# Performance work log

Measured on AMD Instinct MI355X. Metric: run time of the kernel, lower is better.

The kernel has to match this reference:

```python
import jax, jax.numpy as jnp
import numpy as np

N, IN, HID, HEADS, HC, E, K = 50000, 512, 256, 8, 32, 600000, 4
EPS = 1e-5


def _gcn(h_in, W, b, src, dst):
    # PyG GCNConv: add self-loops, symmetric normalization, linear + bias
    h = h_in @ W  # [N, out]
    loop = jnp.arange(N)
    s = jnp.concatenate([src, loop])
    d = jnp.concatenate([dst, loop])
    deg = jax.ops.segment_sum(jnp.ones(s.shape[0], h.dtype), d, num_segments=N)
    dinv = jnp.where(deg > 0, jax.lax.rsqrt(deg), 0.0)
    msg = h[s] * (dinv[s] * dinv[d])[:, None]
    return jax.ops.segment_sum(msg, d, num_segments=N) + b


def _gat(h_in, W, a_src, a_dst, b, src, dst):
    # PyG GATConv: self-loops, LeakyReLU(0.2) logits, per-dst softmax, concat heads
    loop = jnp.arange(N)
    s = jnp.concatenate([src, loop])
    d = jnp.concatenate([dst, loop])
    h = (h_in @ W).reshape(N, HEADS, HC)
    e = jax.nn.leaky_relu((h * a_src).sum(-1)[s] + (h * a_dst).sum(-1)[d], 0.2)  # [E', H]
    m = jax.ops.segment_max(e, d, num_segments=N)  # every node has a self-loop
    ex = jnp.exp(e - m[d])
    alpha = ex / jax.ops.segment_sum(ex, d, num_segments=N)[d]
    out = jax.ops.segment_sum(h[s] * alpha[:, :, None], d, num_segments=N)  # [N, H, C]
    return out.reshape(N, HID) + b


def _ln(h, g, bta):
    mu = h.mean(-1, keepdims=True)
    var = ((h - mu) ** 2).mean(-1, keepdims=True)
    return (h - mu) * jax.lax.rsqrt(var + EPS) * g + bta


def _forward(x, style, stress, params, edges):
    (gW0, gb0, gW1, gb1, gW2, gb2, aW, aas, aad, ab, lg, lb, fW1, fb1, fW2, fb2) = params
    outs = []
    for k in range(K):
        src, dst = edges[k][0], edges[k][1]
        h = jax.nn.relu(_gcn(x, gW0[k], gb0[k], src, dst))
        h = jax.nn.relu(_gcn(h, gW1[k], gb1[k], src, dst))
        h = jax.nn.relu(_gcn(h, gW2[k], gb2[k], src, dst))
        h = _gat(h, aW[k], aas[k], aad[k], ab[k], src, dst)
        outs.append(_ln(h, lg[k], lb[k]))
    ctx = jnp.concatenate([style, stress], axis=-1)
    w = jax.nn.softmax(jnp.tanh(ctx @ fW1 + fb1) @ fW2 + fb2, axis=-1)  # [N, K]
    stacked = jnp.stack(outs, axis=1)  # [N, K, HID]
    return jnp.einsum('nk,nkd->nd', w, stacked)


def setup_inputs() -> dict:
    key = jax.random.key(0)
    ks = jax.random.split(key, 16)
    rn = lambda k, shape, s=0.05: jax.random.normal(k, shape, jnp.float32) * s
    return {
        "x": rn(ks[0], (N, IN), 1.0),
        "style_features": rn(ks[1], (N, HID), 1.0),
        "stress_features": rn(ks[2], (N, HID), 1.0),
        "edge_index0": jax.random.randint(ks[3], (2, E), 0, N),
        "edge_index1": jax.random.randint(ks[4], (2, E), 0, N),
        "edge_index2": jax.random.randint(ks[5], (2, E), 0, N),
        "edge_index3": jax.random.randint(ks[6], (2, E), 0, N),
        "gcn_W0": rn(ks[7], (K, IN, HID)),
        "gcn_b0": jnp.zeros((K, HID), jnp.float32),
        "gcn_W1": rn(ks[8], (K, HID, HID)),
        "gcn_b1": jnp.zeros((K, HID), jnp.float32),
        "gcn_W2": rn(ks[9], (K, HID, HID)),
        "gcn_b2": jnp.zeros((K, HID), jnp.float32),
        "gat_W": rn(ks[10], (K, HID, HID)),
        "gat_a_src": rn(ks[11], (K, HEADS, HC), 0.1),
        "gat_a_dst": rn(ks[12], (K, HEADS, HC), 0.1),
        "gat_b": jnp.zeros((K, HID), jnp.float32),
        "ln_g": jnp.ones((K, HID), jnp.float32),
        "ln_b": jnp.zeros((K, HID), jnp.float32),
        "fus_W1": rn(ks[13], (2 * HID, HID)),
        "fus_b1": jnp.zeros((HID,), jnp.float32),
        "fus_W2": rn(ks[14], (HID, K)),
        "fus_b2": jnp.zeros((K,), jnp.float32),
    }


def reference(x, edge_index0, edge_index1, edge_index2, edge_index3, style_features, stress_features, gcn_W0, gcn_b0, gcn_W1, gcn_b1, gcn_W2, gcn_b2, gat_W, gat_a_src, gat_a_dst, gat_b, ln_g, ln_b, fus_W1, fus_b1, fus_W2, fus_b2):
    params = (gcn_W0, gcn_b0, gcn_W1, gcn_b1, gcn_W2, gcn_b2, gat_W, gat_a_src, gat_a_dst, gat_b, ln_g, ln_b, fus_W1, fus_b1, fus_W2, fus_b2)
    edges = (edge_index0, edge_index1, edge_index2, edge_index3)
    return _forward(x, style_features, stress_features, params, edges)
```

## Files before the change

### kernel.cpp

```cpp
#include <hip/hip_runtime.h>
#include <hip/hip_bf16.h>
#include <cstdint>

#define N_NODES 50000
#define IN_DIM  512
#define HID     256
#define NEDGE   600000
#define TOPO    4
#define DEGMAX  96

typedef __attribute__((ext_vector_type(4))) float floatx4;
typedef _Float16 half4 __attribute__((ext_vector_type(4)));
typedef _Float16 half8 __attribute__((ext_vector_type(8)));

__global__ void conv_f2h_kernel(const float* __restrict__ src, _Float16* __restrict__ dst, int n4) {
  int i = blockIdx.x * 256 + threadIdx.x;
  if (i < n4) {
    float4 v = ((const float4*)src)[i];
    half4 h;
    h[0] = (_Float16)v.x; h[1] = (_Float16)v.y; h[2] = (_Float16)v.z; h[3] = (_Float16)v.w;
    ((half4*)dst)[i] = h;
  }
}

__global__ void conv_ctx_kernel(const float* __restrict__ style, const float* __restrict__ stress,
                                _Float16* __restrict__ dst) {
  int i = blockIdx.x * 256 + threadIdx.x;
  if (i >= N_NODES * 128) return;
  int n = i >> 7, c4 = i & 127;
  int c = c4 * 4;
  const float* s = (c < 256) ? (style + (size_t)n * 256 + c) : (stress + (size_t)n * 256 + (c - 256));
  float4 v = *(const float4*)s;
  half4 h;
  h[0] = (_Float16)v.x; h[1] = (_Float16)v.y; h[2] = (_Float16)v.z; h[3] = (_Float16)v.w;
  ((half4*)(dst + (size_t)n * 512))[c4] = h;
}

#define WT_FUS 0
#define WT_G0  131072
#define WT_G1  655360
#define WT_G2  917504
#define WT_AW  1179648
#define WT_TOT 1441792
__global__ void wconv_all_kernel(const float* __restrict__ fW1, const float* __restrict__ gW0,
                                 const float* __restrict__ gW1, const float* __restrict__ gW2,
                                 const float* __restrict__ aW, _Float16* __restrict__ wt) {
  int idx = blockIdx.x * 256 + threadIdx.x;
  if (idx >= WT_TOT) return;
  const float* src;
  int local, sh;
  if (idx < WT_G0) { src = fW1; sh = 9; local = idx; }
  else if (idx < WT_G1) { int r = idx - WT_G0; src = gW0 + (size_t)(r >> 17) * 131072; sh = 9; local = r & 131071; }
  else if (idx < WT_G2) { int r = idx - WT_G1; src = gW1 + (size_t)(r >> 16) * 65536; sh = 8; local = r & 65535; }
  else if (idx < WT_AW) { int r = idx - WT_G2; src = gW2 + (size_t)(r >> 16) * 65536; sh = 8; local = r & 65535; }
  else { int r = idx - WT_AW; src = aW + (size_t)(r >> 16) * 65536; sh = 8; local = r & 65535; }
  int n = local >> sh;
  int kd = local & ((1 << sh) - 1);
  wt[idx] = (_Float16)src[(size_t)kd * 256 + n];
}

template <int KD>
__global__ __launch_bounds__(256, 3) void gemm_f16_kernel(
    const _Float16* __restrict__ A, const _Float16* __restrict__ Wt,
    const float* __restrict__ bias, _Float16* __restrict__ C, int M, int mode) {
  constexpr int NIT = KD / 32;
  __shared__ __align__(16) _Float16 As[2][2048];
  const int tid = threadIdx.x;
  const int lane = tid & 63;
  const int wv = tid >> 6;
  const int mr = lane & 15;
  const int q = (lane >> 4) & 3;
  const int r0 = blockIdx.x * 64;

  {
  }
  int arow = r0 + ((tid >> 6) * 16) + (tid & 15);
  if (arow > M - 1) arow = M - 1;
  const _Float16* pa = A + (size_t)arow * KD + ((tid >> 4) & 3) * 8;
  const _Float16* pb[4];
#pragma unroll
  for (int t = 0; t < 4; ++t)
    pb[t] = Wt + (size_t)((wv * 4 + t) * 16 + mr) * KD + q * 8;

  floatx4 acc[4][4];
#pragma unroll
  for (int g = 0; g < 4; ++g)
#pragma unroll
    for (int t = 0; t < 4; ++t) acc[g][t] = (floatx4){0.f, 0.f, 0.f, 0.f};

  half8 a0, a1, b0[4], b1[4];
  a0 = *(const half8*)pa; pa += 32;
#pragma unroll
  for (int t = 0; t < 4; ++t) { b0[t] = *(const half8*)pb[t]; pb[t] += 32; }
  *(half8*)&As[0][(unsigned)tid * 8] = a0;
  if (NIT > 1) { a1 = *(const half8*)pa; pa += 32; }
  __syncthreads();

#pragma unroll 1
  for (int it = 0; it < NIT; it += 2) {
    if (it + 1 < NIT) {
      *(half8*)&As[1][(unsigned)tid * 8] = a1;
#pragma unroll
      for (int t = 0; t < 4; ++t) { b1[t] = *(const half8*)pb[t]; pb[t] += 32; }
      if (it + 2 < NIT) { a0 = *(const half8*)pa; pa += 32; }
    }
    {
      half8 af[4];
#pragma unroll
      for (int g = 0; g < 4; ++g) af[g] = *(const half8*)&As[0][(g * 64 + lane) * 8];
#pragma unroll
      for (int g = 0; g < 4; ++g)
#pragma unroll
        for (int t = 0; t < 4; ++t)
          acc[g][t] = __builtin_amdgcn_mfma_f32_16x16x32_f16(b0[t], af[g], acc[g][t], 0, 0, 0);
    }
    if (it + 1 < NIT) {
      __syncthreads();
      if (it + 2 < NIT) {
        *(half8*)&As[0][(unsigned)tid * 8] = a0;
#pragma unroll
        for (int t = 0; t < 4; ++t) { b0[t] = *(const half8*)pb[t]; pb[t] += 32; }
        if (it + 3 < NIT) { a1 = *(const half8*)pa; pa += 32; }
      }
      half8 af[4];
#pragma unroll
      for (int g = 0; g < 4; ++g) af[g] = *(const half8*)&As[1][(g * 64 + lane) * 8];
#pragma unroll
      for (int g = 0; g < 4; ++g)
#pragma unroll
        for (int t = 0; t < 4; ++t)
          acc[g][t] = __builtin_amdgcn_mfma_f32_16x16x32_f16(b1[t], af[g], acc[g][t], 0, 0, 0);
      if (it + 2 < NIT) __syncthreads();
    }
  }

#pragma unroll
  for (int t = 0; t < 4; ++t) {
    int c0 = (wv * 4 + t) * 16 + q * 4;
    float4 bv;
    if (bias) bv = *(const float4*)&bias[c0];
    else { bv.x = 0.f; bv.y = 0.f; bv.z = 0.f; bv.w = 0.f; }
#pragma unroll
    for (int g = 0; g < 4; ++g) {
      int row = r0 + g * 16 + mr;
      if (row < M) {
        half4 o;
#pragma unroll
        for (int r = 0; r < 4; ++r) {
          float v = acc[g][t][r] + (&bv.x)[r];
          if (mode == 1) v = tanhf(v);
          o[r] = (_Float16)v;
        }
        *(half4*)&C[(size_t)row * HID + c0] = o;
      }
    }
  }
}

__global__ void zero_int_kernel(int* p, int n) {
  int i = blockIdx.x * 256 + threadIdx.x;
  if (i < n) p[i] = 0;
}
__global__ void fill_kernel(const int* __restrict__ src, const int* __restrict__ dst,
                            int* __restrict__ cur, int* __restrict__ csr_src, int n) {
  int i = blockIdx.x * 256 + threadIdx.x;
  if (i < n) {
    int d = dst[i];
    int slot = atomicAdd(&cur[d], 1);
    if (slot < DEGMAX) csr_src[(size_t)d * DEGMAX + slot] = src[i];
  }
}
__global__ void dinv_kernel(const int* __restrict__ deg, float* __restrict__ dinv, int n) {
  int i = blockIdx.x * 256 + threadIdx.x;
  if (i < n) dinv[i] = rsqrtf((float)(deg[i] + 1));
}

__global__ __launch_bounds__(256) void gcn_agg_kernel(
    const _Float16* __restrict__ hlin, const int* __restrict__ deg,
    const int* __restrict__ csr_src, const float* __restrict__ dinv,
    const float* __restrict__ bias, _Float16* __restrict__ out) {
  int w = (int)((blockIdx.x * blockDim.x + threadIdx.x) >> 6);
  int lane = threadIdx.x & 63;
  if (w >= N_NODES) return;
  float dv = dinv[w];
  half4 hv = ((const half4*)(hlin + (size_t)w * HID))[lane];
  float sn = dv * dv;
  float A0 = (float)hv[0] * sn, A1 = (float)hv[1] * sn,
        A2 = (float)hv[2] * sn, A3 = (float)hv[3] * sn;
  float B0 = 0.f, B1 = 0.f, B2 = 0.f, B3 = 0.f;
  float C0 = 0.f, C1 = 0.f, C2 = 0.f, C3 = 0.f;
  float D0 = 0.f, D1 = 0.f, D2 = 0.f, D3 = 0.f;
  int dg = deg[w];
  const int* sp = csr_src + (size_t)w * DEGMAX;
  int s = 0;
  for (; s + 4 <= dg; s += 4) {
    int i0 = sp[s], i1 = sp[s + 1], i2 = sp[s + 2], i3 = sp[s + 3];
    float n0 = dinv[i0] * dv, n1 = dinv[i1] * dv, n2 = dinv[i2] * dv, n3 = dinv[i3] * dv;
    half4 v0 = ((const half4*)(hlin + (size_t)i0 * HID))[lane];
    half4 v1 = ((const half4*)(hlin + (size_t)i1 * HID))[lane];
    half4 v2 = ((const half4*)(hlin + (size_t)i2 * HID))[lane];
    half4 v3 = ((const half4*)(hlin + (size_t)i3 * HID))[lane];
    A0 += (float)v0[0] * n0; A1 += (float)v0[1] * n0; A2 += (float)v0[2] * n0; A3 += (float)v0[3] * n0;
    B0 += (float)v1[0] * n1; B1 += (float)v1[1] * n1; B2 += (float)v1[2] * n1; B3 += (float)v1[3] * n1;
    C0 += (float)v2[0] * n2; C1 += (float)v2[1] * n2; C2 += (float)v2[2] * n2; C3 += (float)v2[3] * n2;
    D0 += (float)v3[0] * n3; D1 += (float)v3[1] * n3; D2 += (float)v3[2] * n3; D3 += (float)v3[3] * n3;
  }
  for (; s < dg; ++s) {
    int sc = sp[s];
    float nr = dinv[sc] * dv;
    half4 v = ((const half4*)(hlin + (size_t)sc * HID))[lane];
    A0 += (float)v[0] * nr; A1 += (float)v[1] * nr;
    A2 += (float)v[2] * nr; A3 += (float)v[3] * nr;
  }
  float4 b = ((const float4*)bias)[lane];
  half4 r;
  r[0] = (_Float16)fmaxf(A0 + B0 + C0 + D0 + b.x, 0.f);
  r[1] = (_Float16)fmaxf(A1 + B1 + C1 + D1 + b.y, 0.f);
  r[2] = (_Float16)fmaxf(A2 + B2 + C2 + D2 + b.z, 0.f);
  r[3] = (_Float16)fmaxf(A3 + B3 + C3 + D3 + b.w, 0.f);
  ((half4*)(out + (size_t)w * HID))[lane] = r;
}

__global__ __launch_bounds__(256) void gat_prep_kernel(
    const _Float16* __restrict__ hlin, const float* __restrict__ a_src,
    const float* __restrict__ a_dst, float* __restrict__ asad) {
  int w = (int)((blockIdx.x * blockDim.x + threadIdx.x) >> 6);
  int lane = threadIdx.x & 63;
  if (w >= N_NODES) return;
  half4 h = ((const half4*)(hlin + (size_t)w * HID))[lane];
  float4 s4 = ((const float4*)a_src)[lane];
  float4 d4 = ((const float4*)a_dst)[lane];
  float hx = h[0], hy = h[1], hz = h[2], hw = h[3];
  float ps = hx * s4.x + hy * s4.y + hz * s4.z + hw * s4.w;
  float pd = hx * d4.x + hy * d4.y + hz * d4.z + hw * d4.w;
  for (int o = 1; o < 8; o <<= 1) { ps += __shfl_xor(ps, o, 64); pd += __shfl_xor(pd, o, 64); }
  if ((lane & 7) == 0) {
    int hh = lane >> 3;
    asad[(size_t)w * 16 + hh] = ps;
    asad[(size_t)w * 16 + 8 + hh] = pd;
  }
}

static __device__ __forceinline__ float lrelu(float e) {
  return e > 0.f ? e : 0.2f * e;
}

__global__ __launch_bounds__(256) void gat_agg_kernel(
    const _Float16* __restrict__ hlin, const int* __restrict__ deg,
    const int* __restrict__ csr_src, const float* __restrict__ asad,
    const float* __restrict__ bias, _Float16* __restrict__ out) {
  int w = (int)((blockIdx.x * blockDim.x + threadIdx.x) >> 6);
  int lane = threadIdx.x & 63;
  if (w >= N_NODES) return;
  int head = lane >> 3;
  float ad_d = asad[(size_t)w * 16 + 8 + head];
  float e_self = lrelu(asad[(size_t)w * 16 + head] + ad_d);
  int dg = deg[w];
  const int* sp = csr_src + (size_t)w * DEGMAX;
  float m = e_self;
  {
    int s = 0;
    for (; s + 4 <= dg; s += 4) {
      float e0 = lrelu(asad[(size_t)sp[s] * 16 + head] + ad_d);
      float e1 = lrelu(asad[(size_t)sp[s + 1] * 16 + head] + ad_d);
      float e2 = lrelu(asad[(size_t)sp[s + 2] * 16 + head] + ad_d);
      float e3 = lrelu(asad[(size_t)sp[s + 3] * 16 + head] + ad_d);
      m = fmaxf(m, fmaxf(fmaxf(e0, e1), fmaxf(e2, e3)));
    }
    for (; s < dg; ++s) m = fmaxf(m, lrelu(asad[(size_t)sp[s] * 16 + head] + ad_d));
  }
  float lA = __expf(e_self - m), lB = 0.f, lC = 0.f, lD = 0.f;
  half4 hv = ((const half4*)(hlin + (size_t)w * HID))[lane];
  float A0 = (float)hv[0] * lA, A1 = (float)hv[1] * lA,
        A2 = (float)hv[2] * lA, A3 = (float)hv[3] * lA;
  float B0 = 0.f, B1 = 0.f, B2 = 0.f, B3 = 0.f;
  float C0 = 0.f, C1 = 0.f, C2 = 0.f, C3 = 0.f;
  float D0 = 0.f, D1 = 0.f, D2 = 0.f, D3 = 0.f;
  int s = 0;
  for (; s + 4 <= dg; s += 4) {
    int i0 = sp[s], i1 = sp[s + 1], i2 = sp[s + 2], i3 = sp[s + 3];
    float w0 = __expf(lrelu(asad[(size_t)i0 * 16 + head] + ad_d) - m);
    float w1 = __expf(lrelu(asad[(size_t)i1 * 16 + head] + ad_d) - m);
    float w2 = __expf(lrelu(asad[(size_t)i2 * 16 + head] + ad_d) - m);
    float w3 = __expf(lrelu(asad[(size_t)i3 * 16 + head] + ad_d) - m);
    half4 v0 = ((const half4*)(hlin + (size_t)i0 * HID))[lane];
    half4 v1 = ((const half4*)(hlin + (size_t)i1 * HID))[lane];
    half4 v2 = ((const half4*)(hlin + (size_t)i2 * HID))[lane];
    half4 v3 = ((const half4*)(hlin + (size_t)i3 * HID))[lane];
    lA += w0; lB += w1; lC += w2; lD += w3;
    A0 += (float)v0[0] * w0; A1 += (float)v0[1] * w0; A2 += (float)v0[2] * w0; A3 += (float)v0[3] * w0;
    B0 += (float)v1[0] * w1; B1 += (float)v1[1] * w1; B2 += (float)v1[2] * w1; B3 += (float)v1[3] * w1;
    C0 += (float)v2[0] * w2; C1 += (float)v2[1] * w2; C2 += (float)v2[2] * w2; C3 += (float)v2[3] * w2;
    D0 += (float)v3[0] * w3; D1 += (float)v3[1] * w3; D2 += (float)v3[2] * w3; D3 += (float)v3[3] * w3;
  }
  for (; s < dg; ++s) {
    int sc = sp[s];
    float w0 = __expf(lrelu(asad[(size_t)sc * 16 + head] + ad_d) - m);
    half4 v = ((const half4*)(hlin + (size_t)sc * HID))[lane];
    lA += w0;
    A0 += (float)v[0] * w0; A1 += (float)v[1] * w0;
    A2 += (float)v[2] * w0; A3 += (float)v[3] * w0;
  }
  float inv = 1.f / (lA + lB + lC + lD);
  float4 b = ((const float4*)bias)[lane];
  half4 r;
  r[0] = (_Float16)((A0 + B0 + C0 + D0) * inv + b.x);
  r[1] = (_Float16)((A1 + B1 + C1 + D1) * inv + b.y);
  r[2] = (_Float16)((A2 + B2 + C2 + D2) * inv + b.z);
  r[3] = (_Float16)((A3 + B3 + C3 + D3) * inv + b.w);
  ((half4*)(out + (size_t)w * HID))[lane] = r;
}

__global__ __launch_bounds__(256) void fusw_kernel(
    const _Float16* __restrict__ t, const float* __restrict__ W2,
    const float* __restrict__ b2, float* __restrict__ wout) {
  int w = (int)((blockIdx.x * blockDim.x + threadIdx.x) >> 6);
  int lane = threadIdx.x & 63;
  if (w >= N_NODES) return;
  half4 t4h = ((const half4*)(t + (size_t)w * HID))[lane];
  float tx = t4h[0], ty = t4h[1], tz = t4h[2], tw = t4h[3];
  int c = lane * 4;
  float4 w0 = ((const float4*)W2)[c + 0];
  float4 w1 = ((const float4*)W2)[c + 1];
  float4 w2 = ((const float4*)W2)[c + 2];
  float4 w3 = ((const float4*)W2)[c + 3];
  float p0 = tx * w0.x + ty * w1.x + tz * w2.x + tw * w3.x;
  float p1 = tx * w0.y + ty * w1.y + tz * w2.y + tw * w3.y;
  float p2 = tx * w0.z + ty * w1.z + tz * w2.z + tw * w3.z;
  float p3 = tx * w0.w + ty * w1.w + tz * w2.w + tw * w3.w;
  for (int o = 1; o < 64; o <<= 1) {
    p0 += __shfl_xor(p0, o, 64); p1 += __shfl_xor(p1, o, 64);
    p2 += __shfl_xor(p2, o, 64); p3 += __shfl_xor(p3, o, 64);
  }
  if (lane == 0) {
    p0 += b2[0]; p1 += b2[1]; p2 += b2[2]; p3 += b2[3];
    float mx = fmaxf(fmaxf(p0, p1), fmaxf(p2, p3));
    float e0 = __expf(p0 - mx), e1 = __expf(p1 - mx), e2 = __expf(p2 - mx), e3 = __expf(p3 - mx);
    float inv = 1.f / (e0 + e1 + e2 + e3);
    float4 r; r.x = e0 * inv; r.y = e1 * inv; r.z = e2 * inv; r.w = e3 * inv;
    ((float4*)wout)[w] = r;
  }
}

__global__ __launch_bounds__(256) void ln_acc_kernel(
    const _Float16* __restrict__ hin, const float* __restrict__ g,
    const float* __restrict__ b, const float* __restrict__ wsel, int kk,
    float* __restrict__ dout) {
  int w = (int)((blockIdx.x * blockDim.x + threadIdx.x) >> 6);
  int lane = threadIdx.x & 63;
  if (w >= N_NODES) return;
  half4 v4 = ((const half4*)(hin + (size_t)w * HID))[lane];
  float vx = v4[0], vy = v4[1], vz = v4[2], vw = v4[3];
  float s = vx + vy + vz + vw;
  for (int o = 1; o < 64; o <<= 1) s += __shfl_xor(s, o, 64);
  float mu = s * (1.f / HID);
  float dx = vx - mu, dy = vy - mu, dz = vz - mu, dw = vw - mu;
  float q = dx * dx + dy * dy + dz * dz + dw * dw;
  for (int o = 1; o < 64; o <<= 1) q += __shfl_xor(q, o, 64);
  float rs = rsqrtf(q * (1.f / HID) + 1e-5f);
  float4 g4 = ((const float4*)g)[lane];
  float4 b4 = ((const float4*)b)[lane];
  float wk = wsel[(size_t)w * 4 + kk];
  float4 r;
  r.x = (dx * rs * g4.x + b4.x) * wk;
  r.y = (dy * rs * g4.y + b4.y) * wk;
  r.z = (dz * rs * g4.z + b4.z) * wk;
  r.w = (dw * rs * g4.w + b4.w) * wk;
  float4* dp = (float4*)(dout + (size_t)w * HID) + lane;
  if (kk == 0) {
    *dp = r;
  } else {
    float4 old = *dp;
    old.x += r.x; old.y += r.y; old.z += r.z; old.w += r.w;
    *dp = old;
  }
}

extern "C" void kernel_launch(void* const* d_in, const int* in_sizes, int n_in,
                              void* d_out, int out_size, void* d_ws, size_t ws_size,
                              hipStream_t stream) {
  const float* x      = (const float*)d_in[0];
  const float* style  = (const float*)d_in[1];
  const float* stress = (const float*)d_in[2];
  const int* edges[4] = {(const int*)d_in[3], (const int*)d_in[4],
                         (const int*)d_in[5], (const int*)d_in[6]};
  const float* gW0 = (const float*)d_in[7];
  const float* gb0 = (const float*)d_in[8];
  const float* gW1 = (const float*)d_in[9];
  const float* gb1 = (const float*)d_in[10];
  const float* gW2 = (const float*)d_in[11];
  const float* gb2 = (const float*)d_in[12];
  const float* aW  = (const float*)d_in[13];
  const float* aas = (const float*)d_in[14];
  const float* aad = (const float*)d_in[15];
  const float* ab  = (const float*)d_in[16];
  const float* lg  = (const float*)d_in[17];
  const float* lb  = (const float*)d_in[18];
  const float* fW1 = (const float*)d_in[19];
  const float* fb1 = (const float*)d_in[20];
  const float* fW2 = (const float*)d_in[21];
  const float* fb2 = (const float*)d_in[22];
  float* out = (float*)d_out;
  (void)in_sizes; (void)n_in; (void)out_size; (void)ws_size;

  char* wsp = (char*)d_ws;
  size_t off = 0;
  auto alloc = [&](size_t bytes) -> void* {
    void* p = wsp + off;
    off += (bytes + 255) & ~(size_t)255;
    return p;
  };
  _Float16* h_act = (_Float16*)alloc((size_t)N_NODES * HID * 2);
  _Float16* h_lin = (_Float16*)alloc((size_t)N_NODES * HID * 2);
  _Float16* x_h   = (_Float16*)alloc((size_t)N_NODES * IN_DIM * 2);
  _Float16* wtall = (_Float16*)alloc((size_t)WT_TOT * 2);
  float* wsel = (float*)alloc((size_t)N_NODES * 4 * 4);
  float* dinv = (float*)alloc((size_t)N_NODES * 4);
  int* cur = (int*)alloc((size_t)N_NODES * 4);
  float* asad = (float*)alloc((size_t)N_NODES * 16 * 4);
  char* shared_region = (char*)alloc((size_t)N_NODES * IN_DIM * 2);
  _Float16* ctx_h = (_Float16*)shared_region;
  int* csr_src = (int*)shared_region;

  dim3 blk(256);
  const int nodeWaveBlocks = N_NODES / 4;
  const int nBlocksN = (N_NODES + 255) / 256;
  const int nBlocksE = (NEDGE + 255) / 256;
  const int gemmBlocks = (N_NODES + 63) / 64;

  conv_f2h_kernel<<<(N_NODES * IN_DIM / 4 + 255) / 256, blk, 0, stream>>>(x, x_h, N_NODES * IN_DIM / 4);
  conv_ctx_kernel<<<(N_NODES * 128 + 255) / 256, blk, 0, stream>>>(style, stress, ctx_h);
  wconv_all_kernel<<<(WT_TOT + 255) / 256, blk, 0, stream>>>(fW1, gW0, gW1, gW2, aW, wtall);

  gemm_f16_kernel<512><<<gemmBlocks, blk, 0, stream>>>(ctx_h, wtall + WT_FUS, fb1, h_lin, N_NODES, 1);
  fusw_kernel<<<nodeWaveBlocks, blk, 0, stream>>>(h_lin, fW2, fb2, wsel);

  for (int k = 0; k < TOPO; ++k) {
    const int* srcp = edges[k];
    const int* dstp = edges[k] + NEDGE;
    zero_int_kernel<<<nBlocksN, blk, 0, stream>>>(cur, N_NODES);
    fill_kernel<<<nBlocksE, blk, 0, stream>>>(srcp, dstp, cur, csr_src, NEDGE);
    dinv_kernel<<<nBlocksN, blk, 0, stream>>>(cur, dinv, N_NODES);

    gemm_f16_kernel<512><<<gemmBlocks, blk, 0, stream>>>(
        x_h, wtall + WT_G0 + (size_t)k * 131072, nullptr, h_lin, N_NODES, 0);
    gcn_agg_kernel<<<nodeWaveBlocks, blk, 0, stream>>>(h_lin, cur, csr_src, dinv,
                                                       gb0 + (size_t)k * HID, h_act);
    gemm_f16_kernel<256><<<gemmBlocks, blk, 0, stream>>>(
        h_act, wtall + WT_G1 + (size_t)k * 65536, nullptr, h_lin, N_NODES, 0);
    gcn_agg_kernel<<<nodeWaveBlocks, blk, 0, stream>>>(h_lin, cur, csr_src, dinv,
                                                       gb1 + (size_t)k * HID, h_act);
    gemm_f16_kernel<256><<<gemmBlocks, blk, 0, stream>>>(
        h_act, wtall + WT_G2 + (size_t)k * 65536, nullptr, h_lin, N_NODES, 0);
    gcn_agg_kernel<<<nodeWaveBlocks, blk, 0, stream>>>(h_lin, cur, csr_src, dinv,
                                                       gb2 + (size_t)k * HID, h_act);
    gemm_f16_kernel<256><<<gemmBlocks, blk, 0, stream>>>(
        h_act, wtall + WT_AW + (size_t)k * 65536, nullptr, h_lin, N_NODES, 0);
    gat_prep_kernel<<<nodeWaveBlocks, blk, 0, stream>>>(h_lin, aas + (size_t)k * HID,
                                                        aad + (size_t)k * HID, asad);
    gat_agg_kernel<<<nodeWaveBlocks, blk, 0, stream>>>(h_lin, cur, csr_src, asad,
                                                       ab + (size_t)k * HID, h_act);
    ln_acc_kernel<<<nodeWaveBlocks, blk, 0, stream>>>(h_act, lg + (size_t)k * HID,
                                                      lb + (size_t)k * HID, wsel, k, out);
  }
}
```

Baseline: 2.002 ms.

## Fold GCN normalization into GEMM epilogue, fuse LayerNorm into GAT, use global-max softmax bound

Source-side dinv scaling moves into the GEMM epilogue, so GCN aggregation no longer gathers dinv per neighbor and applies the destination scale once at the end. The GAT softmax's per-node max pass over neighbors is replaced by an upper bound built from a global per-head max of source logits, computed by a new small reduction kernel with ordered-uint atomics. LayerNorm and the weighted accumulation are fused into the GAT aggregation kernel, which removes one kernel and a round trip of the activations. Neighbor indices are now loaded as int4, and degree is clamped to DEGMAX. The global-max bound risks exp underflow when a node's logits sit far below the global maximum.

```diff
diff --git a/kernel.cpp b/kernel.cpp
--- a/kernel.cpp
+++ b/kernel.cpp
@@ -12,6 +12,15 @@
 typedef __attribute__((ext_vector_type(4))) float floatx4;
 typedef _Float16 half4 __attribute__((ext_vector_type(4)));
 typedef _Float16 half8 __attribute__((ext_vector_type(8)));
+
+static __device__ __forceinline__ unsigned f2ord(float f) {
+  unsigned b = __float_as_uint(f);
+  return (b & 0x80000000u) ? ~b : (b | 0x80000000u);
+}
+static __device__ __forceinline__ float ord2f(unsigned u) {
+  unsigned b = (u & 0x80000000u) ? (u & 0x7fffffffu) : ~u;
+  return __uint_as_float(b);
+}
 
 __global__ void conv_f2h_kernel(const float* __restrict__ src, _Float16* __restrict__ dst, int n4) {
   int i = blockIdx.x * 256 + threadIdx.x;
@@ -62,7 +71,8 @@
 template <int KD>
 __global__ __launch_bounds__(256, 3) void gemm_f16_kernel(
     const _Float16* __restrict__ A, const _Float16* __restrict__ Wt,
-    const float* __restrict__ bias, _Float16* __restrict__ C, int M, int mode) {
+    const float* __restrict__ bias, _Float16* __restrict__ C, int M, int mode,
+    const float* __restrict__ scale) {
   constexpr int NIT = KD / 32;
   __shared__ __align__(16) _Float16 As[2][2048];
   const int tid = threadIdx.x;
@@ -72,8 +82,6 @@
   const int q = (lane >> 4) & 3;
   const int r0 = blockIdx.x * 64;
 
-  {
-  }
   int arow = r0 + ((tid >> 6) * 16) + (tid & 15);
   if (arow > M - 1) arow = M - 1;
   const _Float16* pa = A + (size_t)arow * KD + ((tid >> 4) & 3) * 8;
@@ -134,6 +142,12 @@
     }
   }
 
+  float sv[4];
+#pragma unroll
+  for (int g = 0; g < 4; ++g) {
+    int row = r0 + g * 16 + mr;
+    sv[g] = (scale && row < M) ? scale[row] : 1.f;
+  }
 #pragma unroll
   for (int t = 0; t < 4; ++t) {
     int c0 = (wv * 4 + t) * 16 + q * 4;
@@ -149,6 +163,7 @@
         for (int r = 0; r < 4; ++r) {
           float v = acc[g][t][r] + (&bv.x)[r];
           if (mode == 1) v = tanhf(v);
+          v *= sv[g];
           o[r] = (_Float16)v;
         }
         *(half4*)&C[(size_t)row * HID + c0] = o;
@@ -157,9 +172,10 @@
   }
 }
 
-__global__ void zero_int_kernel(int* p, int n) {
+__global__ void zero_int_kernel(int* p, int n, unsigned* gmax) {
   int i = blockIdx.x * 256 + threadIdx.x;
   if (i < n) p[i] = 0;
+  if (blockIdx.x == 0 && threadIdx.x < 8) gmax[threadIdx.x] = 0u;
 }
 __global__ void fill_kernel(const int* __restrict__ src, const int* __restrict__ dst,
                             int* __restrict__ cur, int* __restrict__ csr_src, int n) {
@@ -184,40 +200,35 @@
   if (w >= N_NODES) return;
   float dv = dinv[w];
   half4 hv = ((const half4*)(hlin + (size_t)w * HID))[lane];
-  float sn = dv * dv;
-  float A0 = (float)hv[0] * sn, A1 = (float)hv[1] * sn,
-        A2 = (float)hv[2] * sn, A3 = (float)hv[3] * sn;
+  float A0 = (float)hv[0], A1 = (float)hv[1], A2 = (float)hv[2], A3 = (float)hv[3];
   float B0 = 0.f, B1 = 0.f, B2 = 0.f, B3 = 0.f;
   float C0 = 0.f, C1 = 0.f, C2 = 0.f, C3 = 0.f;
   float D0 = 0.f, D1 = 0.f, D2 = 0.f, D3 = 0.f;
   int dg = deg[w];
+  if (dg > DEGMAX) dg = DEGMAX;
   const int* sp = csr_src + (size_t)w * DEGMAX;
   int s = 0;
   for (; s + 4 <= dg; s += 4) {
-    int i0 = sp[s], i1 = sp[s + 1], i2 = sp[s + 2], i3 = sp[s + 3];
-    float n0 = dinv[i0] * dv, n1 = dinv[i1] * dv, n2 = dinv[i2] * dv, n3 = dinv[i3] * dv;
-    half4 v0 = ((const half4*)(hlin + (size_t)i0 * HID))[lane];
-    half4 v1 = ((const half4*)(hlin + (size_t)i1 * HID))[lane];
-    half4 v2 = ((const half4*)(hlin + (size_t)i2 * HID))[lane];
-    half4 v3 = ((const half4*)(hlin + (size_t)i3 * HID))[lane];
-    A0 += (float)v0[0] * n0; A1 += (float)v0[1] * n0; A2 += (float)v0[2] * n0; A3 += (float)v0[3] * n0;
-    B0 += (float)v1[0] * n1; B1 += (float)v1[1] * n1; B2 += (float)v1[2] * n1; B3 += (float)v1[3] * n1;
-    C0 += (float)v2[0] * n2; C1 += (float)v2[1] * n2; C2 += (float)v2[2] * n2; C3 += (float)v2[3] * n2;
-    D0 += (float)v3[0] * n3; D1 += (float)v3[1] * n3; D2 += (float)v3[2] * n3; D3 += (float)v3[3] * n3;
+    int4 iv = *(const int4*)(sp + s);
+    half4 v0 = ((const half4*)(hlin + (size_t)iv.x * HID))[lane];
+    half4 v1 = ((const half4*)(hlin + (size_t)iv.y * HID))[lane];
+    half4 v2 = ((const half4*)(hlin + (size_t)iv.z * HID))[lane];
+    half4 v3 = ((const half4*)(hlin + (size_t)iv.w * HID))[lane];
+    A0 += (float)v0[0]; A1 += (float)v0[1]; A2 += (float)v0[2]; A3 += (float)v0[3];
+    B0 += (float)v1[0]; B1 += (float)v1[1]; B2 += (float)v1[2]; B3 += (float)v1[3];
+    C0 += (float)v2[0]; C1 += (float)v2[1]; C2 += (float)v2[2]; C3 += (float)v2[3];
+    D0 += (float)v3[0]; D1 += (float)v3[1]; D2 += (float)v3[2]; D3 += (float)v3[3];
   }
   for (; s < dg; ++s) {
-    int sc = sp[s];
-    float nr = dinv[sc] * dv;
-    half4 v = ((const half4*)(hlin + (size_t)sc * HID))[lane];
-    A0 += (float)v[0] * nr; A1 += (float)v[1] * nr;
-    A2 += (float)v[2] * nr; A3 += (float)v[3] * nr;
+    half4 v = ((const half4*)(hlin + (size_t)sp[s] * HID))[lane];
+    A0 += (float)v[0]; A1 += (float)v[1]; A2 += (float)v[2]; A3 += (float)v[3];
   }
   float4 b = ((const float4*)bias)[lane];
   half4 r;
-  r[0] = (_Float16)fmaxf(A0 + B0 + C0 + D0 + b.x, 0.f);
-  r[1] = (_Float16)fmaxf(A1 + B1 + C1 + D1 + b.y, 0.f);
-  r[2] = (_Float16)fmaxf(A2 + B2 + C2 + D2 + b.z, 0.f);
-  r[3] = (_Float16)fmaxf(A3 + B3 + C3 + D3 + b.w, 0.f);
+  r[0] = (_Float16)fmaxf((A0 + B0 + C0 + D0) * dv + b.x, 0.f);
+  r[1] = (_Float16)fmaxf((A1 + B1 + C1 + D1) * dv + b.y, 0.f);
+  r[2] = (_Float16)fmaxf((A2 + B2 + C2 + D2) * dv + b.z, 0.f);
+  r[3] = (_Float16)fmaxf((A3 + B3 + C3 + D3) * dv + b.w, 0.f);
   ((half4*)(out + (size_t)w * HID))[lane] = r;
 }
 
@@ -241,6 +252,19 @@
   }
 }
 
+__global__ __launch_bounds__(256) void gmax_kernel(const float* __restrict__ asad,
+                                                   unsigned* __restrict__ gmax) {
+  int t = threadIdx.x;
+  int h = t & 7;
+  float m = -1e30f;
+  for (int n = blockIdx.x * 32 + (t >> 3); n < N_NODES; n += gridDim.x * 32)
+    m = fmaxf(m, asad[(size_t)n * 16 + h]);
+  m = fmaxf(m, __shfl_xor(m, 8, 64));
+  m = fmaxf(m, __shfl_xor(m, 16, 64));
+  m = fmaxf(m, __shfl_xor(m, 32, 64));
+  if ((t & 63) < 8) atomicMax(&gmax[h], f2ord(m));
+}
+
 static __device__ __forceinline__ float lrelu(float e) {
   return e > 0.f ? e : 0.2f * e;
 }
@@ -248,27 +272,19 @@
 __global__ __launch_bounds__(256) void gat_agg_kernel(
     const _Float16* __restrict__ hlin, const int* __restrict__ deg,
     const int* __restrict__ csr_src, const float* __restrict__ asad,
-    const float* __restrict__ bias, _Float16* __restrict__ out) {
+    const unsigned* __restrict__ gmax, const float* __restrict__ bias,
+    const float* __restrict__ lng, const float* __restrict__ lnb,
+    const float* __restrict__ wsel, int kk, float* __restrict__ dout) {
   int w = (int)((blockIdx.x * blockDim.x + threadIdx.x) >> 6);
   int lane = threadIdx.x & 63;
   if (w >= N_NODES) return;
   int head = lane >> 3;
   float ad_d = asad[(size_t)w * 16 + 8 + head];
+  float m = lrelu(ord2f(gmax[head]) + ad_d);
   float e_self = lrelu(asad[(size_t)w * 16 + head] + ad_d);
   int dg = deg[w];
+  if (dg > DEGMAX) dg = DEGMAX;
   const int* sp = csr_src + (size_t)w * DEGMAX;
-  float m = e_self;
-  {
-    int s = 0;
-    for (; s + 4 <= dg; s += 4) {
-      float e0 = lrelu(asad[(size_t)sp[s] * 16 + head] + ad_d);
-      float e1 = lrelu(asad[(size_t)sp[s + 1] * 16 + head] + ad_d);
-      float e2 = lrelu(asad[(size_t)sp[s + 2] * 16 + head] + ad_d);
-      float e3 = lrelu(asad[(size_t)sp[s + 3] * 16 + head] + ad_d);
-      m = fmaxf(m, fmaxf(fmaxf(e0, e1), fmaxf(e2, e3)));
-    }
-    for (; s < dg; ++s) m = fmaxf(m, lrelu(asad[(size_t)sp[s] * 16 + head] + ad_d));
-  }
   float lA = __expf(e_self - m), lB = 0.f, lC = 0.f, lD = 0.f;
   half4 hv = ((const half4*)(hlin + (size_t)w * HID))[lane];
   float A0 = (float)hv[0] * lA, A1 = (float)hv[1] * lA,
@@ -278,15 +294,15 @@
   float D0 = 0.f, D1 = 0.f, D2 = 0.f, D3 = 0.f;
   int s = 0;
   for (; s + 4 <= dg; s += 4) {
-    int i0 = sp[s], i1 = sp[s + 1], i2 = sp[s + 2], i3 = sp[s + 3];
-    float w0 = __expf(lrelu(asad[(size_t)i0 * 16 + head] + ad_d) - m);
-    float w1 = __expf(lrelu(asad[(size_t)i1 * 16 + head] + ad_d) - m);
-    float w2 = __expf(lrelu(asad[(size_t)i2 * 16 + head] + ad_d) - m);
-    float w3 = __expf(lrelu(asad[(size_t)i3 * 16 + head] + ad_d) - m);
-    half4 v0 = ((const half4*)(hlin + (size_t)i0 * HID))[lane];
-    half4 v1 = ((const half4*)(hlin + (size_t)i1 * HID))[lane];
-    half4 v2 = ((const half4*)(hlin + (size_t)i2 * HID))[lane];
-    half4 v3 = ((const half4*)(hlin + (size_t)i3 * HID))[lane];
+    int4 iv = *(const int4*)(sp + s);
+    float w0 = __expf(lrelu(asad[(size_t)iv.x * 16 + head] + ad_d) - m);
+    float w1 = __expf(lrelu(asad[(size_t)iv.y * 16 + head] + ad_d) - m);
+    float w2 = __expf(lrelu(asad[(size_t)iv.z * 16 + head] + ad_d) - m);
+    float w3 = __expf(lrelu(asad[(size_t)iv.w * 16 + head] + ad_d) - m);
+    half4 v0 = ((const half4*)(hlin + (size_t)iv.x * HID))[lane];
+    half4 v1 = ((const half4*)(hlin + (size_t)iv.y * HID))[lane];
+    half4 v2 = ((const half4*)(hlin + (size_t)iv.z * HID))[lane];
+    half4 v3 = ((const half4*)(hlin + (size_t)iv.w * HID))[lane];
     lA += w0; lB += w1; lC += w2; lD += w3;
     A0 += (float)v0[0] * w0; A1 += (float)v0[1] * w0; A2 += (float)v0[2] * w0; A3 += (float)v0[3] * w0;
     B0 += (float)v1[0] * w1; B1 += (float)v1[1] * w1; B2 += (float)v1[2] * w1; B3 += (float)v1[3] * w1;
@@ -303,12 +319,33 @@
   }
   float inv = 1.f / (lA + lB + lC + lD);
   float4 b = ((const float4*)bias)[lane];
-  half4 r;
-  r[0] = (_Float16)((A0 + B0 + C0 + D0) * inv + b.x);
-  r[1] = (_Float16)((A1 + B1 + C1 + D1) * inv + b.y);
-  r[2] = (_Float16)((A2 + B2 + C2 + D2) * inv + b.z);
-  r[3] = (_Float16)((A3 + B3 + C3 + D3) * inv + b.w);
-  ((half4*)(out + (size_t)w * HID))[lane] = r;
+  float vx = (A0 + B0 + C0 + D0) * inv + b.x;
+  float vy = (A1 + B1 + C1 + D1) * inv + b.y;
+  float vz = (A2 + B2 + C2 + D2) * inv + b.z;
+  float vw = (A3 + B3 + C3 + D3) * inv + b.w;
+  float ssum = vx + vy + vz + vw;
+  for (int o = 1; o < 64; o <<= 1) ssum += __shfl_xor(ssum, o, 64);
+  float mu = ssum * (1.f / HID);
+  float dx = vx - mu, dy = vy - mu, dz = vz - mu, dw = vw - mu;
+  float qq = dx * dx + dy * dy + dz * dz + dw * dw;
+  for (int o = 1; o < 64; o <<= 1) qq += __shfl_xor(qq, o, 64);
+  float rs = rsqrtf(qq * (1.f / HID) + 1e-5f);
+  float4 g4 = ((const float4*)lng)[lane];
+  float4 b4 = ((const float4*)lnb)[lane];
+  float wk = wsel[(size_t)w * 4 + kk];
+  float4 r;
+  r.x = (dx * rs * g4.x + b4.x) * wk;
+  r.y = (dy * rs * g4.y + b4.y) * wk;
+  r.z = (dz * rs * g4.z + b4.z) * wk;
+  r.w = (dw * rs * g4.w + b4.w) * wk;
+  float4* dp = (float4*)(dout + (size_t)w * HID) + lane;
+  if (kk == 0) {
+    *dp = r;
+  } else {
+    float4 old = *dp;
+    old.x += r.x; old.y += r.y; old.z += r.z; old.w += r.w;
+    *dp = old;
+  }
 }
 
 __global__ __launch_bounds__(256) void fusw_kernel(
@@ -339,40 +376,6 @@
     float inv = 1.f / (e0 + e1 + e2 + e3);
     float4 r; r.x = e0 * inv; r.y = e1 * inv; r.z = e2 * inv; r.w = e3 * inv;
     ((float4*)wout)[w] = r;
-  }
-}
-
-__global__ __launch_bounds__(256) void ln_acc_kernel(
-    const _Float16* __restrict__ hin, const float* __restrict__ g,
-    const float* __restrict__ b, const float* __restrict__ wsel, int kk,
-    float* __restrict__ dout) {
-  int w = (int)((blockIdx.x * blockDim.x + threadIdx.x) >> 6);
-  int lane = threadIdx.x & 63;
-  if (w >= N_NODES) return;
-  half4 v4 = ((const half4*)(hin + (size_t)w * HID))[lane];
-  float vx = v4[0], vy = v4[1], vz = v4[2], vw = v4[3];
-  float s = vx + vy + vz + vw;
-  for (int o = 1; o < 64; o <<= 1) s += __shfl_xor(s, o, 64);
-  float mu = s * (1.f / HID);
-  float dx = vx - mu, dy = vy - mu, dz = vz - mu, dw = vw - mu;
-  float q = dx * dx + dy * dy + dz * dz + dw * dw;
-  for (int o = 1; o < 64; o <<= 1) q += __shfl_xor(q, o, 64);
-  float rs = rsqrtf(q * (1.f / HID) + 1e-5f);
-  float4 g4 = ((const float4*)g)[lane];
-  float4 b4 = ((const float4*)b)[lane];
-  float wk = wsel[(size_t)w * 4 + kk];
-  float4 r;
-  r.x = (dx * rs * g4.x + b4.x) * wk;
-  r.y = (dy * rs * g4.y + b4.y) * wk;
-  r.z = (dz * rs * g4.z + b4.z) * wk;
-  r.w = (dw * rs * g4.w + b4.w) * wk;
-  float4* dp = (float4*)(dout + (size_t)w * HID) + lane;
-  if (kk == 0) {
-    *dp = r;
-  } else {
-    float4 old = *dp;
-    old.x += r.x; old.y += r.y; old.z += r.z; old.w += r.w;
-    *dp = old;
   }
 }
 
@@ -418,6 +421,7 @@
   float* dinv = (float*)alloc((size_t)N_NODES * 4);
   int* cur = (int*)alloc((size_t)N_NODES * 4);
   float* asad = (float*)alloc((size_t)N_NODES * 16 * 4);
+  unsigned* gmax = (unsigned*)alloc(256);
   char* shared_region = (char*)alloc((size_t)N_NODES * IN_DIM * 2);
   _Float16* ctx_h = (_Float16*)shared_region;
   int* csr_src = (int*)shared_region;
@@ -432,35 +436,37 @@
   conv_ctx_kernel<<<(N_NODES * 128 + 255) / 256, blk, 0, stream>>>(style, stress, ctx_h);
   wconv_all_kernel<<<(WT_TOT + 255) / 256, blk, 0, stream>>>(fW1, gW0, gW1, gW2, aW, wtall);
 
-  gemm_f16_kernel<512><<<gemmBlocks, blk, 0, stream>>>(ctx_h, wtall + WT_FUS, fb1, h_lin, N_NODES, 1);
+  gemm_f16_kernel<512><<<gemmBlocks, blk, 0, stream>>>(ctx_h, wtall + WT_FUS, fb1, h_lin, N_NODES, 1, nullptr);
   fusw_kernel<<<nodeWaveBlocks, blk, 0, stream>>>(h_lin, fW2, fb2, wsel);
 
   for (int k = 0; k < TOPO; ++k) {
     const int* srcp = edges[k];
     const int* dstp = edges[k] + NEDGE;
-    zero_int_kernel<<<nBlocksN, blk, 0, stream>>>(cur, N_NODES);
+    zero_int_kernel<<<nBlocksN, blk, 0, stream>>>(cur, N_NODES, gmax);
     fill_kernel<<<nBlocksE, blk, 0, stream>>>(srcp, dstp, cur, csr_src, NEDGE);
     dinv_kernel<<<nBlocksN, blk, 0, stream>>>(cur, dinv, N_NODES);
 
     gemm_f16_kernel<512><<<gemmBlocks, blk, 0, stream>>>(
-        x_h, wtall + WT_G0 + (size_t)k * 131072, nullptr, h_lin, N_NODES, 0);
+        x_h, wtall + WT_G0 + (size_t)k * 131072, nullptr, h_lin, N_NODES, 0, dinv);
     gcn_agg_kernel<<<nodeWaveBlocks, blk, 0, stream>>>(h_lin, cur, csr_src, dinv,
                                                        gb0 + (size_t)k * HID, h_act);
     gemm_f16_kernel<256><<<gemmBlocks, blk, 0, stream>>>(
-        h_act, wtall + WT_G1 + (size_t)k * 65536, nullptr, h_lin, N_NODES, 0);
+        h_act, wtall + WT_G1 + (size_t)k * 65536, nullptr, h_lin, N_NODES, 0, dinv);
     gcn_agg_kernel<<<nodeWaveBlocks, blk, 0, stream>>>(h_lin, cur, csr_src, dinv,
                                                        gb1 + (size_t)k * HID, h_act);
     gemm_f16_kernel<256><<<gemmBlocks, blk, 0, stream>>>(
-        h_act, wtall + WT_G2 + (size_t)k * 65536, nullptr, h_lin, N_NODES, 0);
+        h_act, wtall + WT_G2 + (size_t)k * 65536, nullptr, h_lin, N_NODES, 0, dinv);
     gcn_agg_kernel<<<nodeWaveBlocks, blk, 0, stream>>>(h_lin, cur, csr_src, dinv,
                                                        gb2 + (size_t)k * HID, h_act);
     gemm_f16_kernel<256><<<gemmBlocks, blk, 0, stream>>>(
-        h_act, wtall + WT_AW + (size_t)k * 65536, nullptr, h_lin, N_NODES, 0);
+        h_act, wtall + WT_AW + (size_t)k * 65536, nullptr, h_lin, N_NODES, 0, nullptr);
     gat_prep_kernel<<<nodeWaveBlocks, blk, 0, stream>>>(h_lin, aas + (size_t)k * HID,
                                                         aad + (size_t)k * HID, asad);
-    gat_agg_kernel<<<nodeWaveBlocks, blk, 0, stream>>>(h_lin, cur, csr_src, asad,
-                                                       ab + (size_t)k * HID, h_act);
-    ln_acc_kernel<<<nodeWaveBlocks, blk, 0, stream>>>(h_act, lg + (size_t)k * HID,
-                                                      lb + (size_t)k * HID, wsel, k, out);
-  }
-}
+    gmax_kernel<<<64, blk, 0, stream>>>(asad, gmax);
+    gat_agg_kernel<<<nodeWaveBlocks, blk, 0, stream>>>(h_lin, cur, csr_src, asad, gmax,
+                                                       ab + (size_t)k * HID,
+                                                       lg + (size_t)k * HID,
+                                                       lb + (size_t)k * HID,
+                                                       wsel, k, out);
+  }
+}
```

New measurement: 1.950 ms. 2.6% less time.
